# Kernel optimization log

Measured on AMD Instinct MI355X. Metric: run time of the kernel, lower is better.

## Reference

```python
import jax, jax.numpy as jnp
import numpy as np

FS = 30.0          # sampling frequency (Hz)
HIGH_PASS = 40.0   # BPM
LOW_PASS = 250.0   # BPM


def _band_idx(delta_t):
    # static band-pass bin selection (mirrors CalculateNormPSD)
    F = delta_t // 2 + 1
    freqs = np.linspace(0.0, FS / 2.0, F)
    mask = (freqs >= HIGH_PASS / 60.0) & (freqs <= LOW_PASS / 60.0)
    return np.nonzero(mask)[0]


def setup_inputs() -> dict:
    key = jax.random.key(0)
    k1, k2 = jax.random.split(key)
    B, M, T, K, DT = 2, 2048, 4096, 16, 150
    model_output = jax.random.normal(k1, (B, M, T), dtype=jnp.float32)
    offsets = jax.random.randint(k2, (B, M, K), 0, T - DT + 1)
    return {"model_output": model_output, "offsets": offsets, "delta_t": DT}


def reference(model_output, offsets, delta_t):
    B, M, T = model_output.shape
    K = offsets.shape[-1]
    # gather K random segments of length delta_t per (video, location)
    idx = offsets[..., None] + jnp.arange(delta_t)                    # (B,M,K,dt)
    src = jnp.broadcast_to(model_output[:, :, None, :], (B, M, K, T))
    segs = jnp.take_along_axis(src, idx, axis=-1)                     # (B,M,K,dt)
    # normalized PSD (CalculateNormPSD, zero_pad=0)
    segs = segs - jnp.mean(segs, axis=-1, keepdims=True)
    X = jnp.fft.rfft(segs, axis=-1) / delta_t                         # norm='forward'
    psd = X.real ** 2 + X.imag ** 2                                   # (B,M,K,F)
    band = _band_idx(delta_t)
    psd = psd[..., band]
    psd = psd / jnp.sum(psd, axis=-1, keepdims=True)                  # (B,M,K,Fb)
    Fb = psd.shape[-1]
    N = M * K
    S = psd.reshape(B, N, Fb)
    A, Bm = S[0], S[1]

    def pair_sum(P, Q):
        # sum_{i,j} mean_f (P_i - Q_j)^2, closed form
        t = (Q.shape[0] * jnp.sum(P ** 2) + P.shape[0] * jnp.sum(Q ** 2)
             - 2.0 * jnp.dot(jnp.sum(P, axis=0), jnp.sum(Q, axis=0)))
        return t / Fb

    # exclude_same: diagonal (i==j) terms are exactly zero, so they drop out
    self_a = pair_sum(A, A) / (N * (N - 1))
    self_b = pair_sum(Bm, Bm) / (N * (N - 1))
    pos_loss_1 = (self_a + self_b) / 2.0
    pos_loss_2 = pair_sum(A, Bm) / (N * N)
    return pos_loss_1 + pos_loss_2
```

## Files before the change

kernel.cpp:

```cpp
#include <hip/hip_runtime.h>
#include <stdint.h>


#define T_LEN 4096
#define KSEG 16
#define NROWS 4096
#define DTLEN 150
#define NBIN 17
#define SEG_STRIDE 154

__device__ __constant__ float C2TAB[18] = {
  1.9719921f, 1.9562952f, 1.9371663f, 1.9146390f, 1.8887527f, 1.8595530f,
  1.8270909f, 1.7914235f, 1.7526134f, 1.7107286f, 1.6658425f, 1.6180340f,
  1.5673869f, 1.5139901f, 1.4579372f, 1.3993267f, 1.3382612f, 1.2748480f
};

__device__ __forceinline__ void gload_lds(const float* g, float* l) {
  __builtin_amdgcn_global_load_lds(
      (const __attribute__((address_space(1))) void*)g,
      (__attribute__((address_space(3))) void*)l,
      4, 0, 0);
}

__global__ __launch_bounds__(64) void psd_partials(const float* __restrict__ mo,
                                                   const int* __restrict__ offs,
                                                   float* __restrict__ ws) {
  __shared__ float tile[KSEG * SEG_STRIDE];

  const int r = blockIdx.x;
  const int t = threadIdx.x;
  const int seg = t >> 2;
  const int g = t & 3;

  const int off = offs[r * KSEG + seg];
  const float* __restrict__ rowp = mo + (size_t)r * T_LEN;

  #pragma unroll
  for (int s = 0; s < KSEG; ++s) {
    const int off_s = __shfl(off, s << 2, 64);
    const float* src = rowp + off_s;
    float* dst = &tile[s * SEG_STRIDE];
    gload_lds(src + t, dst);
    gload_lds(src + 64 + t, dst + 64);
    if (t < DTLEN - 128) gload_lds(src + 128 + t, dst + 128);
  }
  __syncthreads();

  const int boff = (g == 0) ? 0 : (1 + 4 * g);
  float c[5], s1[5], s2[5];
  #pragma unroll
  for (int j = 0; j < 5; ++j) {
    c[j] = C2TAB[boff + j];
    s1[j] = 0.0f;
    s2[j] = 0.0f;
  }

  const float* __restrict__ x = &tile[seg * SEG_STRIDE];
  #pragma unroll 5
  for (int n = 0; n < DTLEN; n += 2) {
    float x0 = x[n];
    float x1 = x[n + 1];
    #pragma unroll
    for (int j = 0; j < 5; ++j) {
      s2[j] = fmaf(c[j], s1[j], x0 - s2[j]);
      s1[j] = fmaf(c[j], s2[j], x1 - s1[j]);
    }
  }

  float p[5];
  #pragma unroll
  for (int j = 0; j < 5; ++j)
    p[j] = fmaf(s1[j], s1[j], s2[j] * s2[j]) - c[j] * s1[j] * s2[j];
  if (g != 0) p[4] = 0.0f;

  float bs = p[0] + p[1] + p[2] + p[3] + p[4];
  bs += __shfl_xor(bs, 1, 64);
  bs += __shfl_xor(bs, 2, 64);
  const float inv = 1.0f / bs;
  #pragma unroll
  for (int j = 0; j < 5; ++j) p[j] *= inv;

  float ssq = p[0]*p[0] + p[1]*p[1] + p[2]*p[2] + p[3]*p[3] + p[4]*p[4];
  #pragma unroll
  for (int m = 1; m <= 32; m <<= 1) ssq += __shfl_xor(ssq, m, 64);

  #pragma unroll
  for (int m = 4; m <= 32; m <<= 1) {
    #pragma unroll
    for (int j = 0; j < 5; ++j) p[j] += __shfl_xor(p[j], m, 64);
  }

  if (t == 0) ws[r] = ssq;
  if (t < 4) {
    const int nb = (t == 0) ? 5 : 4;
    #pragma unroll
    for (int j = 0; j < 5; ++j)
      if (j < nb) ws[(1 + boff + j) * NROWS + r] = p[j];
  }
}

__global__ __launch_bounds__(1024) void reduce_final(const float* __restrict__ ws,
                                                     float* __restrict__ out) {
  __shared__ double fin[36];
  const int t = threadIdx.x;
  const int w = t >> 6, lane = t & 63;

  for (int p = w; p < 36; p += 16) {
    const float4* __restrict__ base =
        (const float4*)(ws + (p >> 1) * NROWS + (p & 1) * 2048);
    double a = 0.0;
    #pragma unroll
    for (int q = 0; q < 8; ++q) {
      float4 f = base[lane + 64 * q];
      a += (double)f.x + (double)f.y + (double)f.z + (double)f.w;
    }
    #pragma unroll
    for (int m = 32; m >= 1; m >>= 1) a += __shfl_xor(a, m, 64);
    if (lane == 0) fin[p] = a;
  }
  __syncthreads();

  if (t == 0) {
    double sumA2 = fin[0], sumB2 = fin[1];
    double dAA = 0.0, dBB = 0.0, dAB = 0.0;
    #pragma unroll
    for (int f = 0; f < NBIN; ++f) {
      double ca = fin[2 * (1 + f)];
      double cb = fin[2 * (1 + f) + 1];
      dAA += ca * ca;
      dBB += cb * cb;
      dAB += ca * cb;
    }
    const double N = 32768.0;
    const double invFb   = 1.0 / 17.0;
    const double invNN1  = 1.0 / (32768.0 * 32767.0);
    const double invNN   = 1.0 / (32768.0 * 32768.0);
    double pAA = (2.0 * N * sumA2 - 2.0 * dAA) * invFb;
    double pBB = (2.0 * N * sumB2 - 2.0 * dBB) * invFb;
    double pAB = (N * sumA2 + N * sumB2 - 2.0 * dAB) * invFb;
    double selfa = pAA * invNN1;
    double selfb = pBB * invNN1;
    out[0] = (float)(0.5 * (selfa + selfb) + pAB * invNN);
  }
}

extern "C" void kernel_launch(void* const* d_in, const int* in_sizes, int n_in,
                              void* d_out, int out_size, void* d_ws, size_t ws_size,
                              hipStream_t stream) {
  const float* mo = (const float*)d_in[0];
  const int* offs = (const int*)d_in[1];
  float* out = (float*)d_out;
  float* ws = (float*)d_ws;

  psd_partials<<<NROWS, 64, 0, stream>>>(mo, offs, ws);
  reduce_final<<<1, 1024, 0, stream>>>(ws, out);
}
```

Before: 22.02 us.

## Use 16-byte aligned global-to-LDS loads and packed float2 Goertzel recurrences

Segment loads now use 16-byte global_load_lds transfers from a 4-float-aligned base, one instruction per segment instead of three 4-byte ones. The compute loop then reads from the tile at the misalignment offset. The Goertzel recurrences are packed into two-wide vectors so the compiler can emit packed FMA instructions. The LDS stride grows slightly, and each segment loads a few extra elements to cover the misalignment.

```diff
diff --git a/kernel.cpp b/kernel.cpp
--- a/kernel.cpp
+++ b/kernel.cpp
@@ -7,7 +7,9 @@
 #define NROWS 4096
 #define DTLEN 150
 #define NBIN 17
-#define SEG_STRIDE 154
+#define SEG_STRIDE 156
+
+typedef float v2f __attribute__((ext_vector_type(2)));
 
 __device__ __constant__ float C2TAB[18] = {
   1.9719921f, 1.9562952f, 1.9371663f, 1.9146390f, 1.8887527f, 1.8595530f,
@@ -15,11 +17,11 @@
   1.5673869f, 1.5139901f, 1.4579372f, 1.3993267f, 1.3382612f, 1.2748480f
 };
 
-__device__ __forceinline__ void gload_lds(const float* g, float* l) {
+__device__ __forceinline__ void gload_lds16(const float* g, float* l) {
   __builtin_amdgcn_global_load_lds(
       (const __attribute__((address_space(1))) void*)g,
       (__attribute__((address_space(3))) void*)l,
-      4, 0, 0);
+      16, 0, 0);
 }
 
 __global__ __launch_bounds__(64) void psd_partials(const float* __restrict__ mo,
@@ -38,40 +40,41 @@
   #pragma unroll
   for (int s = 0; s < KSEG; ++s) {
     const int off_s = __shfl(off, s << 2, 64);
-    const float* src = rowp + off_s;
-    float* dst = &tile[s * SEG_STRIDE];
-    gload_lds(src + t, dst);
-    gload_lds(src + 64 + t, dst + 64);
-    if (t < DTLEN - 128) gload_lds(src + 128 + t, dst + 128);
+    const int al = off_s & ~3;
+    const int bound = 37 + ((off_s & 3) == 3);
+    if (t <= bound)
+      gload_lds16(rowp + al + 4 * t, &tile[s * SEG_STRIDE]);
   }
   __syncthreads();
 
   const int boff = (g == 0) ? 0 : (1 + 4 * g);
-  float c[5], s1[5], s2[5];
-  #pragma unroll
-  for (int j = 0; j < 5; ++j) {
-    c[j] = C2TAB[boff + j];
-    s1[j] = 0.0f;
-    s2[j] = 0.0f;
+  const v2f c01 = {C2TAB[boff], C2TAB[boff + 1]};
+  const v2f c23 = {C2TAB[boff + 2], C2TAB[boff + 3]};
+  const float c4 = C2TAB[boff + 4];
+
+  v2f a01 = {0.f, 0.f}, a23 = {0.f, 0.f}, b01 = {0.f, 0.f}, b23 = {0.f, 0.f};
+  float a4 = 0.f, b4 = 0.f;
+
+  const float* __restrict__ x = &tile[seg * SEG_STRIDE + (off & 3)];
+  #pragma unroll 5
+  for (int n = 0; n < DTLEN; n += 2) {
+    const float x0 = x[n];
+    const float x1 = x[n + 1];
+    const v2f x0v = {x0, x0};
+    const v2f x1v = {x1, x1};
+    b01 = __builtin_elementwise_fma(c01, a01, x0v - b01);
+    b23 = __builtin_elementwise_fma(c23, a23, x0v - b23);
+    b4  = fmaf(c4, a4, x0 - b4);
+    a01 = __builtin_elementwise_fma(c01, b01, x1v - a01);
+    a23 = __builtin_elementwise_fma(c23, b23, x1v - a23);
+    a4  = fmaf(c4, b4, x1 - a4);
   }
 
-  const float* __restrict__ x = &tile[seg * SEG_STRIDE];
-  #pragma unroll 5
-  for (int n = 0; n < DTLEN; n += 2) {
-    float x0 = x[n];
-    float x1 = x[n + 1];
-    #pragma unroll
-    for (int j = 0; j < 5; ++j) {
-      s2[j] = fmaf(c[j], s1[j], x0 - s2[j]);
-      s1[j] = fmaf(c[j], s2[j], x1 - s1[j]);
-    }
-  }
-
+  const v2f p01 = __builtin_elementwise_fma(a01, a01, b01 * b01) - c01 * (a01 * b01);
+  const v2f p23 = __builtin_elementwise_fma(a23, a23, b23 * b23) - c23 * (a23 * b23);
   float p[5];
-  #pragma unroll
-  for (int j = 0; j < 5; ++j)
-    p[j] = fmaf(s1[j], s1[j], s2[j] * s2[j]) - c[j] * s1[j] * s2[j];
-  if (g != 0) p[4] = 0.0f;
+  p[0] = p01.x; p[1] = p01.y; p[2] = p23.x; p[3] = p23.y;
+  p[4] = (g == 0) ? (fmaf(a4, a4, b4 * b4) - c4 * a4 * b4) : 0.0f;
 
   float bs = p[0] + p[1] + p[2] + p[3] + p[4];
   bs += __shfl_xor(bs, 1, 64);
```

New measurement: 21.79 us. About the same (-1.1%).

## Assign one segment per thread with packed-FP32 Goertzel across all bins

Applied to the files above, without the earlier changes.

Each block now handles four rows (64 segments), with one thread per segment computing all 17 band bins. The Goertzel recurrences use two-wide float vectors so the compiler can emit packed FMA, and LDS reads are software-pipelined in chunks of ten. This removes the cross-lane bin-sum shuffles and uses a quarter as many blocks. In exchange each thread carries more registers and a larger LDS tile (about 39 KB), which lowers occupancy. The 153-float slot stride may also cause LDS bank conflicts when threads read their own segments.

```diff
diff --git a/kernel.cpp b/kernel.cpp
--- a/kernel.cpp
+++ b/kernel.cpp
@@ -7,15 +7,17 @@
 #define NROWS 4096
 #define DTLEN 150
 #define NBIN 17
-#define SEG_STRIDE 154
+#define SEG_SLOT 153
 
-__device__ __constant__ float C2TAB[18] = {
+typedef float v2f __attribute__((ext_vector_type(2)));
+
+__device__ __constant__ float C2TAB[17] = {
   1.9719921f, 1.9562952f, 1.9371663f, 1.9146390f, 1.8887527f, 1.8595530f,
   1.8270909f, 1.7914235f, 1.7526134f, 1.7107286f, 1.6658425f, 1.6180340f,
-  1.5673869f, 1.5139901f, 1.4579372f, 1.3993267f, 1.3382612f, 1.2748480f
+  1.5673869f, 1.5139901f, 1.4579372f, 1.3993267f, 1.3382612f
 };
 
-__device__ __forceinline__ void gload_lds(const float* g, float* l) {
+__device__ __forceinline__ void gload_lds4(const float* g, float* l) {
   __builtin_amdgcn_global_load_lds(
       (const __attribute__((address_space(1))) void*)g,
       (__attribute__((address_space(3))) void*)l,
@@ -25,77 +27,103 @@
 __global__ __launch_bounds__(64) void psd_partials(const float* __restrict__ mo,
                                                    const int* __restrict__ offs,
                                                    float* __restrict__ ws) {
-  __shared__ float tile[KSEG * SEG_STRIDE];
+  __shared__ float tile[64 * SEG_SLOT];
 
-  const int r = blockIdx.x;
+  const int b = blockIdx.x;
   const int t = threadIdx.x;
-  const int seg = t >> 2;
-  const int g = t & 3;
 
-  const int off = offs[r * KSEG + seg];
-  const float* __restrict__ rowp = mo + (size_t)r * T_LEN;
+  const int myoff = offs[(b << 6) + t];
 
   #pragma unroll
-  for (int s = 0; s < KSEG; ++s) {
-    const int off_s = __shfl(off, s << 2, 64);
-    const float* src = rowp + off_s;
-    float* dst = &tile[s * SEG_STRIDE];
-    gload_lds(src + t, dst);
-    gload_lds(src + 64 + t, dst + 64);
-    if (t < DTLEN - 128) gload_lds(src + 128 + t, dst + 128);
+  for (int s = 0; s < 64; ++s) {
+    const int off_s = __shfl(myoff, s, 64);
+    const float* src = mo + ((size_t)((b << 2) + (s >> 4)) << 12) + off_s;
+    float* dst = &tile[s * SEG_SLOT];
+    gload_lds4(src + t, dst);
+    gload_lds4(src + 64 + t, dst + 64);
+    if (t < DTLEN - 128) gload_lds4(src + 128 + t, dst + 128);
   }
   __syncthreads();
 
-  const int boff = (g == 0) ? 0 : (1 + 4 * g);
-  float c[5], s1[5], s2[5];
+  v2f ca[8];
   #pragma unroll
-  for (int j = 0; j < 5; ++j) {
-    c[j] = C2TAB[boff + j];
-    s1[j] = 0.0f;
-    s2[j] = 0.0f;
+  for (int j = 0; j < 8; ++j) ca[j] = (v2f){C2TAB[2 * j], C2TAB[2 * j + 1]};
+  const float c16 = C2TAB[16];
+
+  v2f A[8], Bv[8];
+  #pragma unroll
+  for (int j = 0; j < 8; ++j) { A[j] = (v2f){0.f, 0.f}; Bv[j] = (v2f){0.f, 0.f}; }
+  float A8 = 0.f, B8 = 0.f;
+
+  const float* __restrict__ x = &tile[t * SEG_SLOT];
+
+  float xs[10], xn[10];
+  #pragma unroll
+  for (int q = 0; q < 10; ++q) xs[q] = x[q];
+
+  auto compute10 = [&](const float (&v)[10]) {
+    #pragma unroll
+    for (int q = 0; q < 10; q += 2) {
+      const v2f x0 = {v[q], v[q]};
+      const v2f x1 = {v[q + 1], v[q + 1]};
+      #pragma unroll
+      for (int j = 0; j < 8; ++j)
+        Bv[j] = __builtin_elementwise_fma(ca[j], A[j], x0 - Bv[j]);
+      B8 = fmaf(c16, A8, v[q] - B8);
+      #pragma unroll
+      for (int j = 0; j < 8; ++j)
+        A[j] = __builtin_elementwise_fma(ca[j], Bv[j], x1 - A[j]);
+      A8 = fmaf(c16, B8, v[q + 1] - A8);
+    }
+  };
+
+  #pragma unroll 1
+  for (int it = 0; it < 14; ++it) {
+    #pragma unroll
+    for (int q = 0; q < 10; ++q) xn[q] = x[10 * (it + 1) + q];
+    compute10(xs);
+    #pragma unroll
+    for (int q = 0; q < 10; ++q) xs[q] = xn[q];
+  }
+  compute10(xs);
+
+  v2f P[8];
+  #pragma unroll
+  for (int j = 0; j < 8; ++j) {
+    const v2f ab = A[j] * Bv[j];
+    P[j] = __builtin_elementwise_fma(A[j], A[j], Bv[j] * Bv[j]) - ca[j] * ab;
+  }
+  float p16 = fmaf(A8, A8, B8 * B8) - c16 * A8 * B8;
+
+  v2f acc = P[0] + P[1] + P[2] + P[3] + P[4] + P[5] + P[6] + P[7];
+  const float inv = 1.0f / (acc.x + acc.y + p16);
+  const v2f invv = {inv, inv};
+  #pragma unroll
+  for (int j = 0; j < 8; ++j) P[j] *= invv;
+  p16 *= inv;
+
+  v2f sacc = P[0] * P[0];
+  #pragma unroll
+  for (int j = 1; j < 8; ++j) sacc = __builtin_elementwise_fma(P[j], P[j], sacc);
+  float ssq = fmaf(p16, p16, sacc.x + sacc.y);
+
+  float p[17];
+  #pragma unroll
+  for (int j = 0; j < 8; ++j) { p[2 * j] = P[j].x; p[2 * j + 1] = P[j].y; }
+  p[16] = p16;
+
+  #pragma unroll
+  for (int m = 1; m <= 8; m <<= 1) {
+    ssq += __shfl_xor(ssq, m, 64);
+    #pragma unroll
+    for (int j = 0; j < 17; ++j) p[j] += __shfl_xor(p[j], m, 64);
   }
 
-  const float* __restrict__ x = &tile[seg * SEG_STRIDE];
-  #pragma unroll 5
-  for (int n = 0; n < DTLEN; n += 2) {
-    float x0 = x[n];
-    float x1 = x[n + 1];
+  const int row = (b << 2) + (t >> 4);
+  if ((t & 15) == 0) {
+    ws[row] = ssq;
     #pragma unroll
-    for (int j = 0; j < 5; ++j) {
-      s2[j] = fmaf(c[j], s1[j], x0 - s2[j]);
-      s1[j] = fmaf(c[j], s2[j], x1 - s1[j]);
-    }
-  }
-
-  float p[5];
-  #pragma unroll
-  for (int j = 0; j < 5; ++j)
-    p[j] = fmaf(s1[j], s1[j], s2[j] * s2[j]) - c[j] * s1[j] * s2[j];
-  if (g != 0) p[4] = 0.0f;
-
-  float bs = p[0] + p[1] + p[2] + p[3] + p[4];
-  bs += __shfl_xor(bs, 1, 64);
-  bs += __shfl_xor(bs, 2, 64);
-  const float inv = 1.0f / bs;
-  #pragma unroll
-  for (int j = 0; j < 5; ++j) p[j] *= inv;
-
-  float ssq = p[0]*p[0] + p[1]*p[1] + p[2]*p[2] + p[3]*p[3] + p[4]*p[4];
-  #pragma unroll
-  for (int m = 1; m <= 32; m <<= 1) ssq += __shfl_xor(ssq, m, 64);
-
-  #pragma unroll
-  for (int m = 4; m <= 32; m <<= 1) {
-    #pragma unroll
-    for (int j = 0; j < 5; ++j) p[j] += __shfl_xor(p[j], m, 64);
-  }
-
-  if (t == 0) ws[r] = ssq;
-  if (t < 4) {
-    const int nb = (t == 0) ? 5 : 4;
-    #pragma unroll
-    for (int j = 0; j < 5; ++j)
-      if (j < nb) ws[(1 + boff + j) * NROWS + r] = p[j];
+    for (int e = 0; e < 17; ++e) ws[(1 + e) * NROWS + row] = p[e];
   }
 }
 
@@ -152,6 +180,6 @@
   float* out = (float*)d_out;
   float* ws = (float*)d_ws;
 
-  psd_partials<<<NROWS, 64, 0, stream>>>(mo, offs, ws);
+  psd_partials<<<NROWS / 4, 64, 0, stream>>>(mo, offs, ws);
   reduce_final<<<1, 1024, 0, stream>>>(ws, out);
 }
```

Result: slower. 23.07 us (+4.8%).
